# Kernel optimization log

Measured on AMD Instinct MI355X. Metric: run time of the kernel, lower is better.

Reference implementation:

```python
import jax, jax.numpy as jnp
import numpy as np

N_NODES = 100000
N_EDGES = 1600000
N_FEAT = 64
HIDDEN = 64
N_GRAPHS = 128


def gcn_conv(x, edge_index, W, b, n_nodes):
    # PyG GCNConv defaults: x @ W (no bias), add self-loops, sym-normalize,
    # scatter-add aggregate, then add bias.
    src, dst = edge_index[0], edge_index[1]
    loops = jnp.arange(n_nodes, dtype=src.dtype)
    src = jnp.concatenate([src, loops])
    dst = jnp.concatenate([dst, loops])
    deg = jax.ops.segment_sum(jnp.ones_like(src, dtype=x.dtype), dst,
                              num_segments=n_nodes)
    dinv = jnp.where(deg > 0, jax.lax.rsqrt(jnp.maximum(deg, 1e-12)), 0.0)
    norm = dinv[src] * dinv[dst]                      # [E+N]
    xw = x @ W                                        # [N, H]
    msg = xw[src] * norm[:, None]                     # gather + scale [E+N, H]
    out = jax.ops.segment_sum(msg, dst, num_segments=n_nodes)  # scatter-add
    return out + b


def setup_inputs() -> dict:
    key = jax.random.key(0)
    ks = jax.random.split(key, 12)
    x = jax.random.normal(ks[0], (N_NODES, N_FEAT), dtype=jnp.float32)
    edge_index = jax.random.randint(ks[1], (2, N_EDGES), 0, N_NODES, dtype=jnp.int64)
    batch = jnp.sort(jax.random.randint(ks[2], (N_NODES,), 0, N_GRAPHS, dtype=jnp.int64))
    s = 0.05
    W1 = jax.random.normal(ks[3], (N_FEAT, HIDDEN), dtype=jnp.float32) * s
    b1 = jnp.zeros((HIDDEN,), dtype=jnp.float32)
    W2 = jax.random.normal(ks[4], (HIDDEN, HIDDEN), dtype=jnp.float32) * s
    b2 = jnp.zeros((HIDDEN,), dtype=jnp.float32)
    fc1_w = jax.random.normal(ks[5], (HIDDEN, HIDDEN), dtype=jnp.float32) * s
    fc1_b = jnp.zeros((HIDDEN,), dtype=jnp.float32)
    fc2_w = jax.random.normal(ks[6], (HIDDEN, 1), dtype=jnp.float32) * s
    fc2_b = jnp.zeros((1,), dtype=jnp.float32)
    return {"x": x, "edge_index": edge_index, "batch": batch,
            "W1": W1, "b1": b1, "W2": W2, "b2": b2,
            "fc1_w": fc1_w, "fc1_b": fc1_b, "fc2_w": fc2_w, "fc2_b": fc2_b}


def reference(x, edge_index, batch, W1, b1, W2, b2, fc1_w, fc1_b, fc2_w, fc2_b):
    n = x.shape[0]
    h = jax.nn.relu(gcn_conv(x, edge_index, W1, b1, n))
    h = jax.nn.relu(gcn_conv(h, edge_index, W2, b2, n))
    g = jax.ops.segment_sum(h, batch, num_segments=N_GRAPHS)  # global_add_pool
    g = jax.nn.relu(g @ fc1_w + fc1_b)
    return g @ fc2_w + fc2_b  # [N_GRAPHS, 1]
```

## Files before the change

kernel.cpp:

```cpp
#include <hip/hip_runtime.h>
#include <hip/hip_fp16.h>
#include <hip/hip_fp8.h>


#define NODES_PER_GEMM_BLOCK 16
#define BSHIFT 9
#define NBK_MAX 256
#define EPT 16
#define BCAP 10240
#define GDEPTH 16

union HU2 { uint2 u; __half2 h[2]; };
union HU4 { uint4 u; __half2 h[4]; };

typedef float floatx2 __attribute__((ext_vector_type(2)));

__device__ __forceinline__ int f32x4_to_fp8x4(float a, float b, float c, float d) {
#if __has_builtin(__builtin_amdgcn_cvt_pk_fp8_f32)
    int w = 0;
    w = __builtin_amdgcn_cvt_pk_fp8_f32(a, b, w, false);
    w = __builtin_amdgcn_cvt_pk_fp8_f32(c, d, w, true);
    return w;
#else
    __hip_fp8_e4m3 h0(a), h1(b), h2(c), h3(d);
    return (int)h0.__x | ((int)h1.__x << 8) | ((int)h2.__x << 16) | ((int)h3.__x << 24);
#endif
}

__device__ __forceinline__ void accum8_fp8(float* a, uint2 w, float m) {
#if __has_builtin(__builtin_amdgcn_cvt_pk_f32_fp8)
    floatx2 f01 = __builtin_amdgcn_cvt_pk_f32_fp8(w.x, false);
    floatx2 f23 = __builtin_amdgcn_cvt_pk_f32_fp8(w.x, true);
    floatx2 f45 = __builtin_amdgcn_cvt_pk_f32_fp8(w.y, false);
    floatx2 f67 = __builtin_amdgcn_cvt_pk_f32_fp8(w.y, true);
    a[0] = fmaf(f01[0], m, a[0]); a[1] = fmaf(f01[1], m, a[1]);
    a[2] = fmaf(f23[0], m, a[2]); a[3] = fmaf(f23[1], m, a[3]);
    a[4] = fmaf(f45[0], m, a[4]); a[5] = fmaf(f45[1], m, a[5]);
    a[6] = fmaf(f67[0], m, a[6]); a[7] = fmaf(f67[1], m, a[7]);
#else
    const unsigned char* b = (const unsigned char*)&w;
#pragma unroll
    for (int q = 0; q < 8; ++q) {
        __hip_fp8_e4m3 h; h.__x = b[q];
        a[q] = fmaf((float)h, m, a[q]);
    }
#endif
}

__device__ __forceinline__ void accum8(float* a, const HU4& p, float m) {
#pragma unroll
    for (int q = 0; q < 4; ++q) {
        float2 f = __half22float2(p.h[q]);
        a[2 * q]     = fmaf(f.x, m, a[2 * q]);
        a[2 * q + 1] = fmaf(f.y, m, a[2 * q + 1]);
    }
}

__device__ __forceinline__ void gather_row_fp8(float* acc, const unsigned char* __restrict__ y,
                                               const int* __restrict__ col,
                                               int node, int c8, int beg, int end) {
    uint2 self = *(const uint2*)(y + ((size_t)node << 6) + c8);
    accum8_fp8(acc, self, 1.0f);
    int lim = end - 1;
    for (int j = beg; j < end; j += GDEPTH) {
        uint2 v[GDEPTH];
#pragma unroll
        for (int u = 0; u < GDEPTH; ++u) {
            int p = (j + u <= lim) ? j + u : lim;
            v[u] = *(const uint2*)(y + ((size_t)col[p] << 6) + c8);
        }
#pragma unroll
        for (int u = 0; u < GDEPTH; ++u)
            accum8_fp8(acc, v[u], (j + u <= lim) ? 1.0f : 0.0f);
    }
}

__device__ __forceinline__ void gather_row(float* acc, const __half* __restrict__ y,
                                           const int* __restrict__ col,
                                           int node, int c8, int beg, int end) {
    HU4 self;
    self.u = *(const uint4*)(y + ((size_t)node << 6) + c8);
    accum8(acc, self, 1.0f);
    int lim = end - 1;
    for (int j = beg; j < end; j += GDEPTH) {
        HU4 v[GDEPTH];
#pragma unroll
        for (int u = 0; u < GDEPTH; ++u) {
            int p = (j + u <= lim) ? j + u : lim;
            v[u].u = *(const uint4*)(y + ((size_t)col[p] << 6) + c8);
        }
#pragma unroll
        for (int u = 0; u < GDEPTH; ++u)
            accum8(acc, v[u], (j + u <= lim) ? 1.0f : 0.0f);
    }
}

__global__ void k_binpairs(const int* __restrict__ src, const int* __restrict__ dst,
                           int* __restrict__ bcursor, int* __restrict__ ebuf, int E) {
    __shared__ int cnt[NBK_MAX], base[NBK_MAX];
    int t = threadIdx.x;
    for (int i = t; i < NBK_MAX; i += 256) cnt[i] = 0;
    __syncthreads();
    int e0 = blockIdx.x * (256 * EPT);
    int pk[EPT], bk[EPT];
#pragma unroll
    for (int j = 0; j < EPT; ++j) {
        int e = e0 + j * 256 + t;
        if (e < E) {
            int d = dst[e];
            bk[j] = d >> BSHIFT;
            pk[j] = ((d & 511) << 17) | src[e];
            atomicAdd(&cnt[bk[j]], 1);
        } else bk[j] = -1;
    }
    __syncthreads();
    for (int i = t; i < NBK_MAX; i += 256)
        base[i] = cnt[i] ? atomicAdd(&bcursor[i], cnt[i]) : 0;
    __syncthreads();
    for (int i = t; i < NBK_MAX; i += 256) cnt[i] = 0;
    __syncthreads();
#pragma unroll
    for (int j = 0; j < EPT; ++j) {
        if (bk[j] >= 0) {
            int r = atomicAdd(&cnt[bk[j]], 1);
            ebuf[bk[j] * BCAP + base[bk[j]] + r] = pk[j];
        }
    }
}

__global__ void k_bucket_csr(const int* __restrict__ ebuf, const int* __restrict__ bcnt,
                             int* __restrict__ row_ptr, int* __restrict__ col,
                             float* __restrict__ dinv, int n, int E, int nbk) {
    __shared__ int cnt[512], ofs[512], cur[512];
    __shared__ int ssum[256];
    __shared__ int colBase_s;
    int b = blockIdx.x;
    int t = threadIdx.x;
    int cv = (t < nbk) ? bcnt[t] : 0;
    ssum[t] = cv;
    __syncthreads();
    for (int o = 1; o < 256; o <<= 1) {
        int v = (t >= o) ? ssum[t - o] : 0;
        __syncthreads();
        ssum[t] += v;
        __syncthreads();
    }
    if (t == 0) colBase_s = (b == 0) ? 0 : ssum[b - 1];
    __syncthreads();
    int colBase = colBase_s;
    int myCnt = bcnt[b];
    int nodeBase = b << BSHIFT;
    int nNodes = min(512, n - nodeBase);
    int ebeg = b * BCAP;

    if (b == 0 && t == 0) row_ptr[n] = E;

    cnt[t] = 0; cnt[t + 256] = 0;
    __syncthreads();
    for (int e = t; e < myCnt; e += 256)
        atomicAdd(&cnt[ebuf[ebeg + e] >> 17], 1);
    __syncthreads();
    int a0 = cnt[2 * t], a1 = cnt[2 * t + 1];
    ssum[t] = a0 + a1;
    __syncthreads();
    for (int o = 1; o < 256; o <<= 1) {
        int v = (t >= o) ? ssum[t - o] : 0;
        __syncthreads();
        ssum[t] += v;
        __syncthreads();
    }
    int exc = ssum[t] - (a0 + a1);
    ofs[2 * t] = exc;       ofs[2 * t + 1] = exc + a0;
    cur[2 * t] = exc;       cur[2 * t + 1] = exc + a0;
    __syncthreads();
    for (int i = t; i < nNodes; i += 256) {
        row_ptr[nodeBase + i] = colBase + ofs[i];
        dinv[nodeBase + i] = rsqrtf((float)(cnt[i] + 1));
    }
    __syncthreads();
    for (int e = t; e < myCnt; e += 256) {
        int p = ebuf[ebeg + e];
        int r = atomicAdd(&cur[p >> 17], 1);
        col[colBase + r] = p & 0x1FFFF;
    }
}

__global__ void k_gemm64(const float* __restrict__ in, const float* __restrict__ W,
                         const float* __restrict__ dinv, unsigned char* __restrict__ out,
                         int n) {
    __shared__ float Ws[64 * 64];
    int t = threadIdx.x;
#pragma unroll
    for (int j = 0; j < 4; ++j) {
        int idx = (t + j * 256) * 4;
        *(float4*)&Ws[idx] = *(const float4*)&W[idx];
    }
    __syncthreads();
    int row = blockIdx.x * NODES_PER_GEMM_BLOCK + (t >> 4);
    int c = (t & 15) * 4;
    if (row >= n) return;
    const float* inr = in + (size_t)row * 64;
    float4 acc = make_float4(0.f, 0.f, 0.f, 0.f);
#pragma unroll
    for (int k0 = 0; k0 < 64; k0 += 4) {
        float4 xv = *(const float4*)(inr + k0);
        float xs[4] = {xv.x, xv.y, xv.z, xv.w};
#pragma unroll
        for (int j = 0; j < 4; ++j) {
            float4 w = *(const float4*)&Ws[(k0 + j) * 64 + c];
            acc.x += xs[j] * w.x; acc.y += xs[j] * w.y;
            acc.z += xs[j] * w.z; acc.w += xs[j] * w.w;
        }
    }
    float s = dinv[row];
    int w = f32x4_to_fp8x4(acc.x * s, acc.y * s, acc.z * s, acc.w * s);
    *(int*)(out + ((size_t)row << 6) + c) = w;
}

__global__ void k_gather_gemm(const unsigned char* __restrict__ y, const int* __restrict__ row_ptr,
                              const int* __restrict__ col, const float* __restrict__ dinv,
                              const float* __restrict__ bias, const float* __restrict__ W,
                              __half* __restrict__ out, int n) {
    __shared__ float Ws[64 * 64];
    __shared__ float rowb[32][72];
    int t = threadIdx.x;
#pragma unroll
    for (int j = 0; j < 4; ++j) {
        int idx = (t + j * 256) * 4;
        *(float4*)&Ws[idx] = *(const float4*)&W[idx];
    }
    int nl = t >> 3;
    int node = blockIdx.x * 32 + nl;
    int c8 = (t & 7) * 8;
    bool active = node < n;
    float dn = 0.f;
    if (active) {
        float acc[8] = {0.f, 0.f, 0.f, 0.f, 0.f, 0.f, 0.f, 0.f};
        int beg = row_ptr[node], end = row_ptr[node + 1];
        gather_row_fp8(acc, y, col, node, c8, beg, end);
        dn = dinv[node];
#pragma unroll
        for (int f = 0; f < 8; ++f)
            rowb[nl][c8 + f] = fmaxf(fmaf(acc[f], dn, bias[c8 + f]), 0.f);
    }
    __syncthreads();
    if (!active) return;
    float o[8] = {0.f, 0.f, 0.f, 0.f, 0.f, 0.f, 0.f, 0.f};
#pragma unroll 8
    for (int k = 0; k < 64; ++k) {
        float xk = rowb[nl][k];
        const float* wr = &Ws[k * 64 + c8];
#pragma unroll
        for (int f = 0; f < 8; ++f) o[f] = fmaf(xk, wr[f], o[f]);
    }
    HU4 p;
#pragma unroll
    for (int q = 0; q < 4; ++q)
        p.h[q] = __floats2half2_rn(o[2 * q] * dn, o[2 * q + 1] * dn);
    *(uint4*)(out + ((size_t)node << 6) + c8) = p.u;
}

__global__ void k_gather_pool(const __half* __restrict__ y, const int* __restrict__ row_ptr,
                              const int* __restrict__ col, const float* __restrict__ dinv,
                              const float* __restrict__ bias, const int* __restrict__ batch,
                              float* __restrict__ g, int n) {
    int t = threadIdx.x;
    int blk0 = (int)blockIdx.x * 32;
    int nl = t >> 3;
    int node = blk0 + nl;
    int c8 = (t & 7) * 8;
    __shared__ int bFirst, bLast;
    __shared__ float gl[4 * 64];
    if (t == 0) {
        int i0 = blk0 < n - 1 ? blk0 : n - 1;
        bFirst = batch[i0];
    }
    if (t == 255) {
        int i1 = blk0 + 31 < n - 1 ? blk0 + 31 : n - 1;
        bLast = batch[i1];
    }
    bool active = node < n;
    float h[8] = {0.f, 0.f, 0.f, 0.f, 0.f, 0.f, 0.f, 0.f};
    int bt = 0;
    if (active) {
        float acc[8] = {0.f, 0.f, 0.f, 0.f, 0.f, 0.f, 0.f, 0.f};
        int beg = row_ptr[node], end = row_ptr[node + 1];
        gather_row(acc, y, col, node, c8, beg, end);
        float dn = dinv[node];
#pragma unroll
        for (int f = 0; f < 8; ++f)
            h[f] = fmaxf(fmaf(acc[f], dn, bias[c8 + f]), 0.f);
        bt = batch[node];
    }
    __syncthreads();
    if (bFirst == bLast) {
#pragma unroll
        for (int f = 0; f < 8; ++f) {
            h[f] += __shfl_xor(h[f], 8, 64);
            h[f] += __shfl_xor(h[f], 16, 64);
            h[f] += __shfl_xor(h[f], 32, 64);
        }
        int wv = t >> 6;
        if ((t & 63) < 8) {
#pragma unroll
            for (int f = 0; f < 8; ++f) gl[wv * 64 + (t & 7) * 8 + f] = h[f];
        }
        __syncthreads();
        if (t < 64) {
            float tot = gl[t] + gl[64 + t] + gl[128 + t] + gl[192 + t];
            unsafeAtomicAdd(&g[(size_t)bFirst * 64 + t], tot);
        }
    } else if (active) {
        float* gp = &g[(size_t)bt * 64 + c8];
#pragma unroll
        for (int f = 0; f < 8; ++f) unsafeAtomicAdd(gp + f, h[f]);
    }
}

__global__ void k_head(const float* __restrict__ g, const float* __restrict__ fc1w,
                       const float* __restrict__ fc1b, const float* __restrict__ fc2w,
                       const float* __restrict__ fc2b, float* __restrict__ out) {
    int b = blockIdx.x, t = threadIdx.x;
    __shared__ float gl[64];
    gl[t] = g[(size_t)b * 64 + t];
    __syncthreads();
    float acc = fc1b[t];
#pragma unroll 8
    for (int k = 0; k < 64; ++k) acc += gl[k] * fc1w[k * 64 + t];
    float v = fmaxf(acc, 0.f) * fc2w[t];
#pragma unroll
    for (int o = 32; o > 0; o >>= 1) v += __shfl_down(v, o, 64);
    if (t == 0) out[b] = v + fc2b[0];
}

extern "C" void kernel_launch(void* const* d_in, const int* in_sizes, int n_in,
                              void* d_out, int out_size, void* d_ws, size_t ws_size,
                              hipStream_t stream) {
    const float* x    = (const float*)d_in[0];
    const int*   ei   = (const int*)d_in[1];
    const int*   batch= (const int*)d_in[2];
    const float* W1   = (const float*)d_in[3];
    const float* b1   = (const float*)d_in[4];
    const float* W2   = (const float*)d_in[5];
    const float* b2   = (const float*)d_in[6];
    const float* fc1w = (const float*)d_in[7];
    const float* fc1b = (const float*)d_in[8];
    const float* fc2w = (const float*)d_in[9];
    const float* fc2b = (const float*)d_in[10];
    float* out = (float*)d_out;

    int N = in_sizes[0] / 64;
    int E = in_sizes[1] / 2;
    const int* src = ei;
    const int* dstp = ei + E;
    int G = out_size;
    int nbk = (N + (1 << BSHIFT) - 1) >> BSHIFT;

    float*         base    = (float*)d_ws;
    unsigned char* y1      = (unsigned char*)base;
    float*         scratch = base + (size_t)N * 16;
    int*           ebuf    = (int*)scratch;
    __half*        y2      = (__half*)scratch;
    size_t         scr_w   = (size_t)N * 32;
    float*         dinv    = scratch + scr_w;
    int*           row_ptr = (int*)(dinv + N);
    int*           col     = row_ptr + (N + 1);
    int*           bcursor = col + E;
    float*         g       = (float*)(bcursor + NBK_MAX);

    dim3 blk(256);
    int nb_pairs = (E + 256 * EPT - 1) / (256 * EPT);
    int nb_gemm  = (N + NODES_PER_GEMM_BLOCK - 1) / NODES_PER_GEMM_BLOCK;
    int nb_g32   = (N + 31) / 32;

    hipMemsetAsync(bcursor, 0, (NBK_MAX + (size_t)G * 64) * sizeof(int), stream);

    k_binpairs<<<nb_pairs, blk, 0, stream>>>(src, dstp, bcursor, ebuf, E);
    k_bucket_csr<<<nbk, blk, 0, stream>>>(ebuf, bcursor, row_ptr, col, dinv, N, E, nbk);

    k_gemm64<<<nb_gemm, blk, 0, stream>>>(x, W1, dinv, y1, N);
    k_gather_gemm<<<nb_g32, blk, 0, stream>>>(y1, row_ptr, col, dinv, b1, W2, y2, N);
    k_gather_pool<<<nb_g32, blk, 0, stream>>>(y2, row_ptr, col, dinv, b2, batch, g, N);
    k_head<<<G, 64, 0, stream>>>(g, fc1w, fc1b, fc2w, fc2b, out);
}
```

Measured before the change: 202.3 us.

## Fuse all GCN stages into one cooperative persistent kernel with grid syncs

Replaces the six separate launches and the memset with a single cooperative kernel. It runs each phase (zeroing, edge binning, CSR build, first GEMM, gather+GEMM, gather+pool, head) as a grid-stride loop separated by grid.sync(), and falls back to separate kernels if a cooperative launch is unavailable. The goal is to remove launch overhead and inter-kernel gaps. In exchange, work is capped to a resident grid sized by occupancy, dynamic shared memory is sized for the largest phase (which may lower occupancy), and the gather unroll depth is halved.

```diff
diff --git a/kernel.cpp b/kernel.cpp
--- a/kernel.cpp
+++ b/kernel.cpp
@@ -1,19 +1,30 @@
 #include <hip/hip_runtime.h>
 #include <hip/hip_fp16.h>
 #include <hip/hip_fp8.h>
-
-
-#define NODES_PER_GEMM_BLOCK 16
+#include <hip/hip_cooperative_groups.h>
+
+namespace cg = cooperative_groups;
+
+
 #define BSHIFT 9
 #define NBK_MAX 256
 #define EPT 16
 #define BCAP 10240
-#define GDEPTH 16
-
-union HU2 { uint2 u; __half2 h[2]; };
+#define GDEPTH 8
+#define SMEM_FUSED 25600
+
 union HU4 { uint4 u; __half2 h[4]; };
-
 typedef float floatx2 __attribute__((ext_vector_type(2)));
+
+struct GP {
+    const float* x; const int* src; const int* dst; const int* batch;
+    const float* W1; const float* b1; const float* W2; const float* b2;
+    const float* fc1w; const float* fc1b; const float* fc2w; const float* fc2b;
+    float* out;
+    unsigned char* y1; int* ebuf; __half* y2;
+    float* dinv; int* row_ptr; int* col; int* bcursor; float* g;
+    int N, E, G, nbk;
+};
 
 __device__ __forceinline__ int f32x4_to_fp8x4(float a, float b, float c, float d) {
 #if __has_builtin(__builtin_amdgcn_cvt_pk_fp8_f32)
@@ -95,291 +106,354 @@
     }
 }
 
-__global__ void k_binpairs(const int* __restrict__ src, const int* __restrict__ dst,
-                           int* __restrict__ bcursor, int* __restrict__ ebuf, int E) {
-    __shared__ int cnt[NBK_MAX], base[NBK_MAX];
-    int t = threadIdx.x;
-    for (int i = t; i < NBK_MAX; i += 256) cnt[i] = 0;
-    __syncthreads();
-    int e0 = blockIdx.x * (256 * EPT);
-    int pk[EPT], bk[EPT];
-#pragma unroll
-    for (int j = 0; j < EPT; ++j) {
-        int e = e0 + j * 256 + t;
-        if (e < E) {
-            int d = dst[e];
-            bk[j] = d >> BSHIFT;
-            pk[j] = ((d & 511) << 17) | src[e];
-            atomicAdd(&cnt[bk[j]], 1);
-        } else bk[j] = -1;
-    }
-    __syncthreads();
-    for (int i = t; i < NBK_MAX; i += 256)
-        base[i] = cnt[i] ? atomicAdd(&bcursor[i], cnt[i]) : 0;
-    __syncthreads();
-    for (int i = t; i < NBK_MAX; i += 256) cnt[i] = 0;
-    __syncthreads();
-#pragma unroll
-    for (int j = 0; j < EPT; ++j) {
-        if (bk[j] >= 0) {
-            int r = atomicAdd(&cnt[bk[j]], 1);
-            ebuf[bk[j] * BCAP + base[bk[j]] + r] = pk[j];
-        }
-    }
-}
-
-__global__ void k_bucket_csr(const int* __restrict__ ebuf, const int* __restrict__ bcnt,
-                             int* __restrict__ row_ptr, int* __restrict__ col,
-                             float* __restrict__ dinv, int n, int E, int nbk) {
-    __shared__ int cnt[512], ofs[512], cur[512];
-    __shared__ int ssum[256];
-    __shared__ int colBase_s;
-    int b = blockIdx.x;
-    int t = threadIdx.x;
-    int cv = (t < nbk) ? bcnt[t] : 0;
-    ssum[t] = cv;
-    __syncthreads();
-    for (int o = 1; o < 256; o <<= 1) {
-        int v = (t >= o) ? ssum[t - o] : 0;
-        __syncthreads();
-        ssum[t] += v;
-        __syncthreads();
-    }
-    if (t == 0) colBase_s = (b == 0) ? 0 : ssum[b - 1];
-    __syncthreads();
-    int colBase = colBase_s;
-    int myCnt = bcnt[b];
-    int nodeBase = b << BSHIFT;
-    int nNodes = min(512, n - nodeBase);
-    int ebeg = b * BCAP;
-
-    if (b == 0 && t == 0) row_ptr[n] = E;
-
-    cnt[t] = 0; cnt[t + 256] = 0;
-    __syncthreads();
-    for (int e = t; e < myCnt; e += 256)
-        atomicAdd(&cnt[ebuf[ebeg + e] >> 17], 1);
-    __syncthreads();
-    int a0 = cnt[2 * t], a1 = cnt[2 * t + 1];
-    ssum[t] = a0 + a1;
-    __syncthreads();
-    for (int o = 1; o < 256; o <<= 1) {
-        int v = (t >= o) ? ssum[t - o] : 0;
-        __syncthreads();
-        ssum[t] += v;
-        __syncthreads();
-    }
-    int exc = ssum[t] - (a0 + a1);
-    ofs[2 * t] = exc;       ofs[2 * t + 1] = exc + a0;
-    cur[2 * t] = exc;       cur[2 * t + 1] = exc + a0;
-    __syncthreads();
-    for (int i = t; i < nNodes; i += 256) {
-        row_ptr[nodeBase + i] = colBase + ofs[i];
-        dinv[nodeBase + i] = rsqrtf((float)(cnt[i] + 1));
-    }
-    __syncthreads();
-    for (int e = t; e < myCnt; e += 256) {
-        int p = ebuf[ebeg + e];
-        int r = atomicAdd(&cur[p >> 17], 1);
-        col[colBase + r] = p & 0x1FFFF;
-    }
-}
-
-__global__ void k_gemm64(const float* __restrict__ in, const float* __restrict__ W,
-                         const float* __restrict__ dinv, unsigned char* __restrict__ out,
-                         int n) {
-    __shared__ float Ws[64 * 64];
+
+__device__ void ph_zero(const GP& p) {
+    int tid = blockIdx.x * 256 + threadIdx.x;
+    int stride = gridDim.x * 256;
+    for (int i = tid; i < NBK_MAX; i += stride) p.bcursor[i] = 0;
+    int gw = p.G * 64;
+    for (int i = tid; i < gw; i += stride) p.g[i] = 0.f;
+}
+
+__device__ void ph_binpairs(char* smraw, const GP& p) {
+    int* cnt = (int*)smraw;
+    int* base = cnt + NBK_MAX;
+    int t = threadIdx.x;
+    int nChunk = (p.E + 256 * EPT - 1) / (256 * EPT);
+    for (int ch = blockIdx.x; ch < nChunk; ch += gridDim.x) {
+        for (int i = t; i < NBK_MAX; i += 256) cnt[i] = 0;
+        __syncthreads();
+        int e0 = ch * (256 * EPT);
+        int pk[EPT], bk[EPT];
+#pragma unroll
+        for (int j = 0; j < EPT; ++j) {
+            int e = e0 + j * 256 + t;
+            if (e < p.E) {
+                int d = p.dst[e];
+                bk[j] = d >> BSHIFT;
+                pk[j] = ((d & 511) << 17) | p.src[e];
+                atomicAdd(&cnt[bk[j]], 1);
+            } else bk[j] = -1;
+        }
+        __syncthreads();
+        for (int i = t; i < NBK_MAX; i += 256)
+            base[i] = cnt[i] ? atomicAdd(&p.bcursor[i], cnt[i]) : 0;
+        __syncthreads();
+        for (int i = t; i < NBK_MAX; i += 256) cnt[i] = 0;
+        __syncthreads();
+#pragma unroll
+        for (int j = 0; j < EPT; ++j) {
+            if (bk[j] >= 0) {
+                int r = atomicAdd(&cnt[bk[j]], 1);
+                p.ebuf[bk[j] * BCAP + base[bk[j]] + r] = pk[j];
+            }
+        }
+        __syncthreads();
+    }
+}
+
+__device__ void ph_bucket_csr(char* smraw, const GP& p) {
+    int* cnt = (int*)smraw;
+    int* ofs = cnt + 512;
+    int* cur = ofs + 512;
+    int* ssum = cur + 512;
+    int* colBase_s = ssum + 256;
+    int t = threadIdx.x;
+    if (blockIdx.x == 0 && t == 0) p.row_ptr[p.N] = p.E;
+    for (int b = blockIdx.x; b < p.nbk; b += gridDim.x) {
+        int cv = (t < p.nbk) ? p.bcursor[t] : 0;
+        ssum[t] = cv;
+        __syncthreads();
+        for (int o = 1; o < 256; o <<= 1) {
+            int v = (t >= o) ? ssum[t - o] : 0;
+            __syncthreads();
+            ssum[t] += v;
+            __syncthreads();
+        }
+        if (t == 0) colBase_s[0] = (b == 0) ? 0 : ssum[b - 1];
+        __syncthreads();
+        int colBase = colBase_s[0];
+        int myCnt = p.bcursor[b];
+        int nodeBase = b << BSHIFT;
+        int nNodes = min(512, p.N - nodeBase);
+        int ebeg = b * BCAP;
+        cnt[t] = 0; cnt[t + 256] = 0;
+        __syncthreads();
+        for (int e = t; e < myCnt; e += 256)
+            atomicAdd(&cnt[p.ebuf[ebeg + e] >> 17], 1);
+        __syncthreads();
+        int a0 = cnt[2 * t], a1 = cnt[2 * t + 1];
+        ssum[t] = a0 + a1;
+        __syncthreads();
+        for (int o = 1; o < 256; o <<= 1) {
+            int v = (t >= o) ? ssum[t - o] : 0;
+            __syncthreads();
+            ssum[t] += v;
+            __syncthreads();
+        }
+        int exc = ssum[t] - (a0 + a1);
+        ofs[2 * t] = exc;  ofs[2 * t + 1] = exc + a0;
+        cur[2 * t] = exc;  cur[2 * t + 1] = exc + a0;
+        __syncthreads();
+        for (int i = t; i < nNodes; i += 256) {
+            p.row_ptr[nodeBase + i] = colBase + ofs[i];
+            p.dinv[nodeBase + i] = rsqrtf((float)(cnt[i] + 1));
+        }
+        __syncthreads();
+        for (int e = t; e < myCnt; e += 256) {
+            int pk = p.ebuf[ebeg + e];
+            int r = atomicAdd(&cur[pk >> 17], 1);
+            p.col[colBase + r] = pk & 0x1FFFF;
+        }
+        __syncthreads();
+    }
+}
+
+__device__ void ph_gemm64(char* smraw, const GP& p) {
+    float* Ws = (float*)smraw;
     int t = threadIdx.x;
 #pragma unroll
     for (int j = 0; j < 4; ++j) {
         int idx = (t + j * 256) * 4;
-        *(float4*)&Ws[idx] = *(const float4*)&W[idx];
+        *(float4*)&Ws[idx] = *(const float4*)&p.W1[idx];
     }
     __syncthreads();
-    int row = blockIdx.x * NODES_PER_GEMM_BLOCK + (t >> 4);
-    int c = (t & 15) * 4;
-    if (row >= n) return;
-    const float* inr = in + (size_t)row * 64;
-    float4 acc = make_float4(0.f, 0.f, 0.f, 0.f);
-#pragma unroll
-    for (int k0 = 0; k0 < 64; k0 += 4) {
-        float4 xv = *(const float4*)(inr + k0);
-        float xs[4] = {xv.x, xv.y, xv.z, xv.w};
-#pragma unroll
-        for (int j = 0; j < 4; ++j) {
-            float4 w = *(const float4*)&Ws[(k0 + j) * 64 + c];
-            acc.x += xs[j] * w.x; acc.y += xs[j] * w.y;
-            acc.z += xs[j] * w.z; acc.w += xs[j] * w.w;
-        }
-    }
-    float s = dinv[row];
-    int w = f32x4_to_fp8x4(acc.x * s, acc.y * s, acc.z * s, acc.w * s);
-    *(int*)(out + ((size_t)row << 6) + c) = w;
-}
-
-__global__ void k_gather_gemm(const unsigned char* __restrict__ y, const int* __restrict__ row_ptr,
-                              const int* __restrict__ col, const float* __restrict__ dinv,
-                              const float* __restrict__ bias, const float* __restrict__ W,
-                              __half* __restrict__ out, int n) {
-    __shared__ float Ws[64 * 64];
-    __shared__ float rowb[32][72];
+    int ngrp = (p.N + 15) / 16;
+    int c = (threadIdx.x & 15) * 4;
+    for (int gI = blockIdx.x; gI < ngrp; gI += gridDim.x) {
+        int row = gI * 16 + (t >> 4);
+        if (row < p.N) {
+            const float* inr = p.x + (size_t)row * 64;
+            float4 acc = make_float4(0.f, 0.f, 0.f, 0.f);
+#pragma unroll
+            for (int k0 = 0; k0 < 64; k0 += 4) {
+                float4 xv = *(const float4*)(inr + k0);
+                float xs[4] = {xv.x, xv.y, xv.z, xv.w};
+#pragma unroll
+                for (int j = 0; j < 4; ++j) {
+                    float4 w = *(const float4*)&Ws[(k0 + j) * 64 + c];
+                    acc.x += xs[j] * w.x; acc.y += xs[j] * w.y;
+                    acc.z += xs[j] * w.z; acc.w += xs[j] * w.w;
+                }
+            }
+            float s = p.dinv[row];
+            int w = f32x4_to_fp8x4(acc.x * s, acc.y * s, acc.z * s, acc.w * s);
+            *(int*)(p.y1 + ((size_t)row << 6) + c) = w;
+        }
+    }
+}
+
+__device__ void ph_gather_gemm(char* smraw, const GP& p) {
+    float* Ws = (float*)smraw;
+    float (*rowb)[72] = (float(*)[72])(smraw + 16384);
     int t = threadIdx.x;
 #pragma unroll
     for (int j = 0; j < 4; ++j) {
         int idx = (t + j * 256) * 4;
-        *(float4*)&Ws[idx] = *(const float4*)&W[idx];
+        *(float4*)&Ws[idx] = *(const float4*)&p.W2[idx];
     }
     int nl = t >> 3;
-    int node = blockIdx.x * 32 + nl;
     int c8 = (t & 7) * 8;
-    bool active = node < n;
-    float dn = 0.f;
-    if (active) {
-        float acc[8] = {0.f, 0.f, 0.f, 0.f, 0.f, 0.f, 0.f, 0.f};
-        int beg = row_ptr[node], end = row_ptr[node + 1];
-        gather_row_fp8(acc, y, col, node, c8, beg, end);
-        dn = dinv[node];
-#pragma unroll
-        for (int f = 0; f < 8; ++f)
-            rowb[nl][c8 + f] = fmaxf(fmaf(acc[f], dn, bias[c8 + f]), 0.f);
-    }
-    __syncthreads();
-    if (!active) return;
-    float o[8] = {0.f, 0.f, 0.f, 0.f, 0.f, 0.f, 0.f, 0.f};
+    int ngrp = (p.N + 31) / 32;
+    for (int gI = blockIdx.x; gI < ngrp; gI += gridDim.x) {
+        int node = gI * 32 + nl;
+        bool active = node < p.N;
+        float dn = 0.f;
+        __syncthreads();
+        if (active) {
+            float acc[8] = {0.f, 0.f, 0.f, 0.f, 0.f, 0.f, 0.f, 0.f};
+            int beg = p.row_ptr[node], end = p.row_ptr[node + 1];
+            gather_row_fp8(acc, p.y1, p.col, node, c8, beg, end);
+            dn = p.dinv[node];
+#pragma unroll
+            for (int f = 0; f < 8; ++f)
+                rowb[nl][c8 + f] = fmaxf(fmaf(acc[f], dn, p.b1[c8 + f]), 0.f);
+        }
+        __syncthreads();
+        if (active) {
+            float o[8] = {0.f, 0.f, 0.f, 0.f, 0.f, 0.f, 0.f, 0.f};
 #pragma unroll 8
-    for (int k = 0; k < 64; ++k) {
-        float xk = rowb[nl][k];
-        const float* wr = &Ws[k * 64 + c8];
-#pragma unroll
-        for (int f = 0; f < 8; ++f) o[f] = fmaf(xk, wr[f], o[f]);
-    }
-    HU4 p;
-#pragma unroll
-    for (int q = 0; q < 4; ++q)
-        p.h[q] = __floats2half2_rn(o[2 * q] * dn, o[2 * q + 1] * dn);
-    *(uint4*)(out + ((size_t)node << 6) + c8) = p.u;
-}
-
-__global__ void k_gather_pool(const __half* __restrict__ y, const int* __restrict__ row_ptr,
-                              const int* __restrict__ col, const float* __restrict__ dinv,
-                              const float* __restrict__ bias, const int* __restrict__ batch,
-                              float* __restrict__ g, int n) {
-    int t = threadIdx.x;
-    int blk0 = (int)blockIdx.x * 32;
+            for (int k = 0; k < 64; ++k) {
+                float xk = rowb[nl][k];
+                const float* wr = &Ws[k * 64 + c8];
+#pragma unroll
+                for (int f = 0; f < 8; ++f) o[f] = fmaf(xk, wr[f], o[f]);
+            }
+            HU4 q;
+#pragma unroll
+            for (int v = 0; v < 4; ++v)
+                q.h[v] = __floats2half2_rn(o[2 * v] * dn, o[2 * v + 1] * dn);
+            *(uint4*)(p.y2 + ((size_t)node << 6) + c8) = q.u;
+        }
+    }
+}
+
+__device__ void ph_gather_pool(char* smraw, const GP& p) {
+    int* bF = (int*)smraw;
+    int* bL = bF + 1;
+    float* gl = (float*)(bF + 2);
+    int t = threadIdx.x;
     int nl = t >> 3;
-    int node = blk0 + nl;
     int c8 = (t & 7) * 8;
-    __shared__ int bFirst, bLast;
-    __shared__ float gl[4 * 64];
-    if (t == 0) {
-        int i0 = blk0 < n - 1 ? blk0 : n - 1;
-        bFirst = batch[i0];
-    }
-    if (t == 255) {
-        int i1 = blk0 + 31 < n - 1 ? blk0 + 31 : n - 1;
-        bLast = batch[i1];
-    }
-    bool active = node < n;
-    float h[8] = {0.f, 0.f, 0.f, 0.f, 0.f, 0.f, 0.f, 0.f};
-    int bt = 0;
-    if (active) {
-        float acc[8] = {0.f, 0.f, 0.f, 0.f, 0.f, 0.f, 0.f, 0.f};
-        int beg = row_ptr[node], end = row_ptr[node + 1];
-        gather_row(acc, y, col, node, c8, beg, end);
-        float dn = dinv[node];
-#pragma unroll
-        for (int f = 0; f < 8; ++f)
-            h[f] = fmaxf(fmaf(acc[f], dn, bias[c8 + f]), 0.f);
-        bt = batch[node];
-    }
-    __syncthreads();
-    if (bFirst == bLast) {
-#pragma unroll
-        for (int f = 0; f < 8; ++f) {
-            h[f] += __shfl_xor(h[f], 8, 64);
-            h[f] += __shfl_xor(h[f], 16, 64);
-            h[f] += __shfl_xor(h[f], 32, 64);
-        }
-        int wv = t >> 6;
-        if ((t & 63) < 8) {
-#pragma unroll
-            for (int f = 0; f < 8; ++f) gl[wv * 64 + (t & 7) * 8 + f] = h[f];
-        }
+    int ngrp = (p.N + 31) / 32;
+    for (int gI = blockIdx.x; gI < ngrp; gI += gridDim.x) {
+        int blk0 = gI * 32;
+        __syncthreads();
+        if (t == 0) {
+            int i0 = blk0 < p.N - 1 ? blk0 : p.N - 1;
+            *bF = p.batch[i0];
+        }
+        if (t == 255) {
+            int i1 = blk0 + 31 < p.N - 1 ? blk0 + 31 : p.N - 1;
+            *bL = p.batch[i1];
+        }
+        int node = blk0 + nl;
+        bool active = node < p.N;
+        float h[8] = {0.f, 0.f, 0.f, 0.f, 0.f, 0.f, 0.f, 0.f};
+        int bt = 0;
+        if (active) {
+            float acc[8] = {0.f, 0.f, 0.f, 0.f, 0.f, 0.f, 0.f, 0.f};
+            int beg = p.row_ptr[node], end = p.row_ptr[node + 1];
+            gather_row(acc, p.y2, p.col, node, c8, beg, end);
+            float dn = p.dinv[node];
+#pragma unroll
+            for (int f = 0; f < 8; ++f)
+                h[f] = fmaxf(fmaf(acc[f], dn, p.b2[c8 + f]), 0.f);
+            bt = p.batch[node];
+        }
+        __syncthreads();
+        if (*bF == *bL) {
+            int bg = *bF;
+#pragma unroll
+            for (int f = 0; f < 8; ++f) {
+                h[f] += __shfl_xor(h[f], 8, 64);
+                h[f] += __shfl_xor(h[f], 16, 64);
+                h[f] += __shfl_xor(h[f], 32, 64);
+            }
+            int wv = t >> 6;
+            if ((t & 63) < 8) {
+#pragma unroll
+                for (int f = 0; f < 8; ++f) gl[wv * 64 + (t & 7) * 8 + f] = h[f];
+            }
+            __syncthreads();
+            if (t < 64) {
+                float tot = gl[t] + gl[64 + t] + gl[128 + t] + gl[192 + t];
+                unsafeAtomicAdd(&p.g[(size_t)bg * 64 + t], tot);
+            }
+        } else if (active) {
+            float* gp = &p.g[(size_t)bt * 64 + c8];
+#pragma unroll
+            for (int f = 0; f < 8; ++f) unsafeAtomicAdd(gp + f, h[f]);
+        }
+    }
+}
+
+__device__ void ph_head(char* smraw, const GP& p) {
+    float* gl = (float*)smraw;
+    int t = threadIdx.x;
+    for (int b = blockIdx.x; b < p.G; b += gridDim.x) {
+        __syncthreads();
+        if (t < 64) gl[t] = p.g[(size_t)b * 64 + t];
         __syncthreads();
         if (t < 64) {
-            float tot = gl[t] + gl[64 + t] + gl[128 + t] + gl[192 + t];
-            unsafeAtomicAdd(&g[(size_t)bFirst * 64 + t], tot);
-        }
-    } else if (active) {
-        float* gp = &g[(size_t)bt * 64 + c8];
-#pragma unroll
-        for (int f = 0; f < 8; ++f) unsafeAtomicAdd(gp + f, h[f]);
-    }
-}
-
-__global__ void k_head(const float* __restrict__ g, const float* __restrict__ fc1w,
-                       const float* __restrict__ fc1b, const float* __restrict__ fc2w,
-                       const float* __restrict__ fc2b, float* __restrict__ out) {
-    int b = blockIdx.x, t = threadIdx.x;
-    __shared__ float gl[64];
-    gl[t] = g[(size_t)b * 64 + t];
-    __syncthreads();
-    float acc = fc1b[t];
+            float acc = p.fc1b[t];
 #pragma unroll 8
-    for (int k = 0; k < 64; ++k) acc += gl[k] * fc1w[k * 64 + t];
-    float v = fmaxf(acc, 0.f) * fc2w[t];
-#pragma unroll
-    for (int o = 32; o > 0; o >>= 1) v += __shfl_down(v, o, 64);
-    if (t == 0) out[b] = v + fc2b[0];
-}
+            for (int k = 0; k < 64; ++k) acc += gl[k] * p.fc1w[k * 64 + t];
+            float v = fmaxf(acc, 0.f) * p.fc2w[t];
+#pragma unroll
+            for (int o = 32; o > 0; o >>= 1) v += __shfl_down(v, o, 64);
+            if (t == 0) p.out[b] = v + p.fc2b[0];
+        }
+    }
+}
+
+
+__global__ void __launch_bounds__(256) k_fused(GP p) {
+    extern __shared__ char sm[];
+    cg::grid_group grid = cg::this_grid();
+    ph_zero(p);            grid.sync();
+    ph_binpairs(sm, p);    grid.sync();
+    ph_bucket_csr(sm, p);  grid.sync();
+    ph_gemm64(sm, p);      grid.sync();
+    ph_gather_gemm(sm, p); grid.sync();
+    ph_gather_pool(sm, p); grid.sync();
+    ph_head(sm, p);
+}
+
+__global__ void __launch_bounds__(256) k_zero_k(GP p)   { ph_zero(p); }
+__global__ void __launch_bounds__(256) k_binpairs(GP p) { extern __shared__ char sm[]; ph_binpairs(sm, p); }
+__global__ void __launch_bounds__(256) k_bucket(GP p)   { extern __shared__ char sm[]; ph_bucket_csr(sm, p); }
+__global__ void __launch_bounds__(256) k_gemm(GP p)     { extern __shared__ char sm[]; ph_gemm64(sm, p); }
+__global__ void __launch_bounds__(256) k_gg(GP p)       { extern __shared__ char sm[]; ph_gather_gemm(sm, p); }
+__global__ void __launch_bounds__(256) k_gp(GP p)       { extern __shared__ char sm[]; ph_gather_pool(sm, p); }
+__global__ void __launch_bounds__(256) k_hd(GP p)       { extern __shared__ char sm[]; ph_head(sm, p); }
 
 extern "C" void kernel_launch(void* const* d_in, const int* in_sizes, int n_in,
                               void* d_out, int out_size, void* d_ws, size_t ws_size,
                               hipStream_t stream) {
-    const float* x    = (const float*)d_in[0];
-    const int*   ei   = (const int*)d_in[1];
-    const int*   batch= (const int*)d_in[2];
-    const float* W1   = (const float*)d_in[3];
-    const float* b1   = (const float*)d_in[4];
-    const float* W2   = (const float*)d_in[5];
-    const float* b2   = (const float*)d_in[6];
-    const float* fc1w = (const float*)d_in[7];
-    const float* fc1b = (const float*)d_in[8];
-    const float* fc2w = (const float*)d_in[9];
-    const float* fc2b = (const float*)d_in[10];
-    float* out = (float*)d_out;
-
-    int N = in_sizes[0] / 64;
-    int E = in_sizes[1] / 2;
-    const int* src = ei;
-    const int* dstp = ei + E;
-    int G = out_size;
-    int nbk = (N + (1 << BSHIFT) - 1) >> BSHIFT;
-
-    float*         base    = (float*)d_ws;
-    unsigned char* y1      = (unsigned char*)base;
-    float*         scratch = base + (size_t)N * 16;
-    int*           ebuf    = (int*)scratch;
-    __half*        y2      = (__half*)scratch;
-    size_t         scr_w   = (size_t)N * 32;
-    float*         dinv    = scratch + scr_w;
-    int*           row_ptr = (int*)(dinv + N);
-    int*           col     = row_ptr + (N + 1);
-    int*           bcursor = col + E;
-    float*         g       = (float*)(bcursor + NBK_MAX);
-
-    dim3 blk(256);
-    int nb_pairs = (E + 256 * EPT - 1) / (256 * EPT);
-    int nb_gemm  = (N + NODES_PER_GEMM_BLOCK - 1) / NODES_PER_GEMM_BLOCK;
-    int nb_g32   = (N + 31) / 32;
-
-    hipMemsetAsync(bcursor, 0, (NBK_MAX + (size_t)G * 64) * sizeof(int), stream);
-
-    k_binpairs<<<nb_pairs, blk, 0, stream>>>(src, dstp, bcursor, ebuf, E);
-    k_bucket_csr<<<nbk, blk, 0, stream>>>(ebuf, bcursor, row_ptr, col, dinv, N, E, nbk);
-
-    k_gemm64<<<nb_gemm, blk, 0, stream>>>(x, W1, dinv, y1, N);
-    k_gather_gemm<<<nb_g32, blk, 0, stream>>>(y1, row_ptr, col, dinv, b1, W2, y2, N);
-    k_gather_pool<<<nb_g32, blk, 0, stream>>>(y2, row_ptr, col, dinv, b2, batch, g, N);
-    k_head<<<G, 64, 0, stream>>>(g, fc1w, fc1b, fc2w, fc2b, out);
-}
+    GP p;
+    p.x    = (const float*)d_in[0];
+    const int* ei = (const int*)d_in[1];
+    p.batch= (const int*)d_in[2];
+    p.W1   = (const float*)d_in[3];
+    p.b1   = (const float*)d_in[4];
+    p.W2   = (const float*)d_in[5];
+    p.b2   = (const float*)d_in[6];
+    p.fc1w = (const float*)d_in[7];
+    p.fc1b = (const float*)d_in[8];
+    p.fc2w = (const float*)d_in[9];
+    p.fc2b = (const float*)d_in[10];
+    p.out  = (float*)d_out;
+
+    p.N = in_sizes[0] / 64;
+    p.E = in_sizes[1] / 2;
+    p.src = ei;
+    p.dst = ei + p.E;
+    p.G = out_size;
+    p.nbk = (p.N + (1 << BSHIFT) - 1) >> BSHIFT;
+
+    float* base  = (float*)d_ws;
+    p.y1 = (unsigned char*)base;
+    float* scratch = base + (size_t)p.N * 16;
+    p.ebuf = (int*)scratch;
+    p.y2   = (__half*)scratch;
+    size_t scr_w = (size_t)p.N * 32;
+    p.dinv    = scratch + scr_w;
+    p.row_ptr = (int*)(p.dinv + p.N);
+    p.col     = p.row_ptr + (p.N + 1);
+    p.bcursor = p.col + p.E;
+    p.g       = (float*)(p.bcursor + NBK_MAX);
+
+    bool done = false;
+    int dev = 0;
+    (void)hipGetDevice(&dev);
+    int coop = 0;
+    (void)hipDeviceGetAttribute(&coop, hipDeviceAttributeCooperativeLaunch, dev);
+    if (coop) {
+        int occ = 0, cus = 0;
+        (void)hipOccupancyMaxActiveBlocksPerMultiprocessor(&occ, k_fused, 256, SMEM_FUSED);
+        (void)hipDeviceGetAttribute(&cus, hipDeviceAttributeMultiprocessorCount, dev);
+        long nb = (long)occ * (long)cus;
+        if (nb > 0) {
+            if (nb > 2048) nb = 2048;
+            void* args[] = {(void*)&p};
+            hipError_t e = hipLaunchCooperativeKernel((const void*)k_fused, dim3((int)nb),
+                                                      dim3(256), args, SMEM_FUSED, stream);
+            if (e == hipSuccess) done = true;
+            else (void)hipGetLastError();
+        }
+    }
+
+    if (!done) {
+        int nChunk = (p.E + 256 * EPT - 1) / (256 * EPT);
+        int nGemm  = (p.N + 15) / 16;
+        int nG32   = (p.N + 31) / 32;
+        k_zero_k<<<34, 256, 0, stream>>>(p);
+        k_binpairs<<<nChunk, 256, 2048, stream>>>(p);
+        k_bucket<<<p.nbk, 256, 7172, stream>>>(p);
+        k_gemm<<<nGemm, 256, 16384, stream>>>(p);
+        k_gg<<<nG32, 256, 25600, stream>>>(p);
+        k_gp<<<nG32, 256, 1056, stream>>>(p);
+        k_hd<<<p.G, 256, 256, stream>>>(p);
+    }
+}
```

Measured after the change: 556.3 us. 2.75x slower.
